# Kernel tuning notes

Measured on AMD Instinct MI355X. Metric: run time of the kernel, lower is better.

The kernel has to match this reference:

```python
import jax, jax.numpy as jnp
import numpy as np

V, B, L, NG = 50000, 128, 350, 3        # vocab, batch(docs), doc length, n-gram window
D, H, C = 768, 256, 20                  # bert dim, num_hidden, class_num
HEADS, LAYERS, K, ALPHA = 8, 2, 3, 0.15 # GAT heads/layers, diffusion hops k, alpha


def setup_inputs() -> dict:
    rng = np.random.default_rng(0)
    # per-doc graphs: 350 unique word-ids per doc (nodes), n-gram window edges
    node_ids = np.stack([rng.choice(V, L, replace=False) for _ in range(B)]).ravel()
    src_b, dst_b = [], []
    for i in range(L):
        for j in range(max(0, i - NG), min(L, i + NG + 1)):
            src_b.append(i); dst_b.append(j)
    src_b, dst_b = np.asarray(src_b), np.asarray(dst_b)
    off = (np.arange(B) * L)[:, None]
    edge_src = (src_b[None, :] + off).ravel()
    edge_dst = (dst_b[None, :] + off).ravel()
    graph_id = np.repeat(np.arange(B), L)

    ks = jax.random.split(jax.random.key(0), 8)
    f32 = jnp.float32
    return {
        'node_ids': jnp.asarray(node_ids, jnp.int32),
        'edge_src': jnp.asarray(edge_src, jnp.int32),
        'edge_dst': jnp.asarray(edge_dst, jnp.int32),
        'graph_id': jnp.asarray(graph_id, jnp.int32),
        'emb':    (jax.random.normal(ks[0], (V, D), f32) * 0.02),
        'W1':     (jax.random.normal(ks[1], (D, H), f32) / np.sqrt(D)).astype(f32),
        'b1':     jnp.zeros((H,), f32),
        'W2':     (jax.random.normal(ks[2], (H, C), f32) / np.sqrt(H)).astype(f32),
        'b2':     jnp.zeros((C,), f32),
        'gat_W':  (jax.random.normal(ks[3], (LAYERS, HEADS, C, C), f32) / np.sqrt(C)).astype(f32),
        'a_src':  (jax.random.normal(ks[4], (LAYERS, HEADS, C), f32) * 0.1),
        'a_dst':  (jax.random.normal(ks[5], (LAYERS, HEADS, C), f32) * 0.1),
        'w_gate': (jax.random.normal(ks[6], (C,), f32) / np.sqrt(C)).astype(f32),
        'b_gate': jnp.zeros((), f32),
    }


def _gat_layer(h, W, a_s, a_d, src, dst, N):
    # h: [N,C]; W: [Hd,C,C]; a_s/a_d: [Hd,C]
    z = jnp.einsum('nc,hcd->hnd', h, W)                     # [Hd,N,C]
    e = jax.nn.leaky_relu(jnp.einsum('hnd,hd->hn', z, a_s)[:, src]
                          + jnp.einsum('hnd,hd->hn', z, a_d)[:, dst], 0.2)  # [Hd,E]

    def segsoftmax(ev):  # edge softmax over incoming edges at each dst node
        m = jax.ops.segment_max(ev, dst, num_segments=N)
        ex = jnp.exp(ev - m[dst])
        s = jax.ops.segment_sum(ex, dst, num_segments=N)
        return ex / (s[dst] + 1e-9)

    att = jax.vmap(segsoftmax)(e)                           # [Hd,E]

    def diffuse(zh, ah):  # attention diffusion: Z_t = (1-a) A Z_{t-1} + a Z_0
        zt = zh
        for _ in range(K):
            agg = jax.ops.segment_sum(ah[:, None] * zt[src], dst, num_segments=N)
            zt = (1.0 - ALPHA) * agg + ALPHA * zh
        return zt

    out = jax.vmap(diffuse)(z, att)                         # [Hd,N,C]
    return jax.nn.elu(out).mean(axis=0)                     # merge='mean'


def reference(node_ids, edge_src, edge_dst, graph_id, emb, W1, b1, W2, b2,
              gat_W, a_src, a_dst, w_gate, b_gate):
    N = node_ids.shape[0]
    x = emb[node_ids]                                       # [N,768] gather
    x = jax.nn.relu(x @ W1 + b1)                            # linear1 + ReLU
    h = x @ W2 + b2                                         # linear2 -> [N,C]
    for l in range(LAYERS):
        h = _gat_layer(h, gat_W[l], a_src[l], a_dst[l], edge_src, edge_dst, N)
    gate = jax.nn.sigmoid(h @ w_gate + b_gate)[:, None]     # WeightAndSum gate
    return jax.ops.segment_sum(gate * h, graph_id, num_segments=B)  # [B,C]
```

## Files before the change

### kernel.cpp

```cpp
#include <hip/hip_runtime.h>
#include <hip/hip_bf16.h>
#include <cstddef>

#define NB_NODES 44800
#define NDOCS 128
#define DLEN 350
#define DIM 768
#define HID 256
#define NCLS 20
#define NHEADS 8
#define ZROW 352
#define ASTR 800

typedef __bf16 v8bf __attribute__((ext_vector_type(8)));
typedef __bf16 v4bf __attribute__((ext_vector_type(4)));
typedef __bf16 v2bf __attribute__((ext_vector_type(2)));
typedef float v4f __attribute__((ext_vector_type(4)));
typedef float v2f __attribute__((ext_vector_type(2)));

__global__ __launch_bounds__(256) void k_pack(const float* __restrict__ W1,
                                              __bf16* __restrict__ W1P) {
  int idx = blockIdx.x * 256 + threadIdx.x;
  int e = idx & 7;
  int l = (idx >> 3) & 63;
  int rest = idx >> 9;
  int ks = rest % 24;
  int cb = rest / 24;
  int k = ks * 32 + (l >> 4) * 8 + e;
  int col = cb * 16 + (l & 15);
  W1P[idx] = (__bf16)W1[k * 256 + col];
}

__global__ __launch_bounds__(256) void k_mlp(
    const int* __restrict__ node_ids, const float* __restrict__ emb,
    const __bf16* __restrict__ W1P, const float* __restrict__ b1,
    const float* __restrict__ W2, const float* __restrict__ b2,
    float* __restrict__ h0) {
  __shared__ __align__(16) char smem[51200];
  __bf16* Asl = (__bf16*)smem;
  float*  xs  = (float*)smem;
  __bf16* w2s = (__bf16*)(smem + 16640);
  int tid = threadIdx.x;
  int wave = tid >> 6, lane = tid & 63;
  int quad = lane >> 4, l16 = lane & 15;
  int m0 = blockIdx.x * 32;

  {
    int r0 = wave * 8;
    int nid[8];
#pragma unroll
    for (int rr = 0; rr < 8; ++rr) nid[rr] = node_ids[m0 + r0 + rr];
#pragma unroll
    for (int p = 0; p < 3; ++p) {
      v4f t[8];
#pragma unroll
      for (int rr = 0; rr < 8; ++rr)
        t[rr] = *(const v4f*)(emb + (size_t)nid[rr] * DIM + p * 256 + lane * 4);
#pragma unroll
      for (int rr = 0; rr < 8; ++rr) {
        v4bf b;
#pragma unroll
        for (int e = 0; e < 4; ++e) b[e] = (__bf16)t[rr][e];
        *(v4bf*)(Asl + (r0 + rr) * ASTR + p * 256 + lane * 4) = b;
      }
    }
  }

  v4f acc[2][4];
#pragma unroll
  for (int ms = 0; ms < 2; ++ms)
#pragma unroll
    for (int j = 0; j < 4; ++j) acc[ms][j] = (v4f){0.f, 0.f, 0.f, 0.f};

  __syncthreads();

  const __bf16* wpB = W1P + (size_t)wave * 49152 + lane * 8;
#pragma unroll 4
  for (int ks = 0; ks < 24; ++ks) {
    v8bf a0 = *(const v8bf*)(Asl + l16 * ASTR + ks * 32 + quad * 8);
    v8bf a1 = *(const v8bf*)(Asl + (16 + l16) * ASTR + ks * 32 + quad * 8);
    v8bf bv[4];
#pragma unroll
    for (int j = 0; j < 4; ++j)
      bv[j] = *(const v8bf*)(wpB + j * 12288 + ks * 512);
#pragma unroll
    for (int j = 0; j < 4; ++j) {
      acc[0][j] = __builtin_amdgcn_mfma_f32_16x16x32_bf16(a0, bv[j], acc[0][j], 0, 0, 0);
      acc[1][j] = __builtin_amdgcn_mfma_f32_16x16x32_bf16(a1, bv[j], acc[1][j], 0, 0, 0);
    }
  }

  __syncthreads();
  for (int i = tid; i < HID * NCLS; i += 256) w2s[i] = (__bf16)W2[i];

#pragma unroll
  for (int ms = 0; ms < 2; ++ms) {
    if (ms) __syncthreads();
#pragma unroll
    for (int j = 0; j < 4; ++j) {
      int col = wave * 64 + j * 16 + l16;
      float bb = b1[col];
#pragma unroll
      for (int r = 0; r < 4; ++r) {
        int lr = quad * 4 + r;
        float v = acc[ms][j][r] + bb;
        xs[lr * 260 + col] = v > 0.f ? v : 0.f;
      }
    }
    __syncthreads();
    if (tid < 160) {
      int m = tid / 10, c0 = (tid % 10) * 2;
      float s0 = b2[c0], s1 = b2[c0 + 1];
      for (int k = 0; k < HID; ++k) {
        float x = xs[m * 260 + k];
        v2bf w = *(const v2bf*)(w2s + k * NCLS + c0);
        s0 += x * (float)w[0]; s1 += x * (float)w[1];
      }
      v2f o; o[0] = s0; o[1] = s1;
      *(v2f*)(h0 + (size_t)(m0 + ms * 16 + m) * NCLS + c0) = o;
    }
  }
}

__global__ __launch_bounds__(384) void k_gat(
    const float* __restrict__ hin, const float* __restrict__ gatW,
    const float* __restrict__ a_src, const float* __restrict__ a_dst,
    int layer, float* __restrict__ zout) {
  __shared__ float zT[NCLS * ZROW];
  __shared__ float asv[DLEN], adv[DLEN];
  int tid = threadIdx.x;
  int head = blockIdx.x & 7;
  int doc = blockIdx.x >> 3;
  const float* W  = gatW  + (size_t)(layer * NHEADS + head) * NCLS * NCLS;
  const float* av = a_src + (layer * NHEADS + head) * NCLS;
  const float* dv = a_dst + (layer * NHEADS + head) * NCLS;
  int r = tid;
  bool act = r < DLEN;

  float z0[NCLS];
  if (act) {
    const float* hr = hin + ((size_t)doc * DLEN + r) * NCLS;
    float h[NCLS];
#pragma unroll
    for (int q = 0; q < 5; ++q) {
      v4f t = *(const v4f*)(hr + q * 4);
#pragma unroll
      for (int e = 0; e < 4; ++e) h[q * 4 + e] = t[e];
    }
    float zacc[NCLS];
#pragma unroll
    for (int d = 0; d < NCLS; ++d) zacc[d] = 0.f;
#pragma unroll
    for (int c = 0; c < NCLS; ++c) {
      float hc = h[c];
#pragma unroll
      for (int d = 0; d < NCLS; ++d) zacc[d] += hc * W[c * NCLS + d];
    }
    float sa = 0.f, sd = 0.f;
#pragma unroll
    for (int d = 0; d < NCLS; ++d) { sa += zacc[d] * av[d]; sd += zacc[d] * dv[d]; }
    asv[r] = sa; adv[r] = sd;
#pragma unroll
    for (int c = 0; c < NCLS; ++c) zT[c * ZROW + r] = zacc[c];
#pragma unroll
    for (int d = 0; d < NCLS; ++d) z0[d] = zacc[d];
  }
  __syncthreads();

  float att[7];
  if (act) {
    float ad = adv[r];
    float e[7]; float m = -1e30f;
#pragma unroll
    for (int j = 0; j < 7; ++j) {
      int s = r - 3 + j;
      bool valid = (s >= 0) && (s < DLEN);
      float x = valid ? asv[s] + ad : -1e30f;
      x = x > 0.f ? x : 0.2f * x;
      e[j] = valid ? x : -1e30f;
      if (e[j] > m) m = e[j];
    }
    float sum = 0.f;
#pragma unroll
    for (int j = 0; j < 7; ++j) {
      float ex = (e[j] > -1e29f) ? expf(e[j] - m) : 0.f;
      e[j] = ex; sum += ex;
    }
    float inv = 1.f / (sum + 1e-9f);
#pragma unroll
    for (int j = 0; j < 7; ++j) att[j] = e[j] * inv;
  }

  float vn[NCLS];
  for (int hop = 0; hop < 3; ++hop) {
    if (act) {
      float agg[NCLS];
#pragma unroll
      for (int c = 0; c < NCLS; ++c) agg[c] = 0.f;
#pragma unroll
      for (int j = 0; j < 7; ++j) {
        int s = r - 3 + j;
        s = s < 0 ? 0 : (s > DLEN - 1 ? DLEN - 1 : s);
        float a = att[j];
#pragma unroll
        for (int c = 0; c < NCLS; ++c) agg[c] += a * zT[c * ZROW + s];
      }
#pragma unroll
      for (int c = 0; c < NCLS; ++c) vn[c] = 0.85f * agg[c] + 0.15f * z0[c];
    }
    if (hop < 2) {
      __syncthreads();
      if (act) {
#pragma unroll
        for (int c = 0; c < NCLS; ++c) zT[c * ZROW + r] = vn[c];
      }
      __syncthreads();
    }
  }

  if (act) {
    float* og = zout + ((size_t)head * NB_NODES + (size_t)doc * DLEN + r) * NCLS;
#pragma unroll
    for (int q = 0; q < 5; ++q) {
      v4f t;
#pragma unroll
      for (int e = 0; e < 4; ++e) {
        float x = vn[q * 4 + e];
        t[e] = x > 0.f ? x : expf(x) - 1.f;
      }
      *(v4f*)(og + q * 4) = t;
    }
  }
}

__global__ __launch_bounds__(256) void k_headmean(
    const float* __restrict__ eluzt, float* __restrict__ hout) {
  int idx = blockIdx.x * 256 + threadIdx.x;
  v4f s = (v4f){0.f, 0.f, 0.f, 0.f};
#pragma unroll
  for (int h = 0; h < NHEADS; ++h)
    s += ((const v4f*)eluzt)[(size_t)h * (NB_NODES * NCLS / 4) + idx];
  v4f o; o[0] = s[0] * 0.125f; o[1] = s[1] * 0.125f; o[2] = s[2] * 0.125f; o[3] = s[3] * 0.125f;
  ((v4f*)hout)[idx] = o;
}

__global__ __launch_bounds__(384) void k_hm_pool(
    const float* __restrict__ eluzt, const float* __restrict__ w_gate,
    const float* __restrict__ b_gate, float* __restrict__ out) {
  __shared__ float red[6][NCLS];
  int tid = threadIdx.x;
  int doc = blockIdx.x;
  int r = tid;
  bool act = r < DLEN;

  float wg[NCLS];
#pragma unroll
  for (int c = 0; c < NCLS; ++c) wg[c] = w_gate[c];
  float contrib[NCLS];
#pragma unroll
  for (int c = 0; c < NCLS; ++c) contrib[c] = 0.f;
  if (act) {
    float hm[NCLS];
#pragma unroll
    for (int c = 0; c < NCLS; ++c) hm[c] = 0.f;
#pragma unroll
    for (int hd = 0; hd < NHEADS; ++hd) {
      const float* p = eluzt + ((size_t)hd * NB_NODES + (size_t)doc * DLEN + r) * NCLS;
#pragma unroll
      for (int q = 0; q < 5; ++q) {
        v4f t = *(const v4f*)(p + q * 4);
#pragma unroll
        for (int e = 0; e < 4; ++e) hm[q * 4 + e] += t[e];
      }
    }
    float d = b_gate[0];
#pragma unroll
    for (int c = 0; c < NCLS; ++c) { hm[c] *= 0.125f; d += hm[c] * wg[c]; }
    float g = 1.f / (1.f + expf(-d));
#pragma unroll
    for (int c = 0; c < NCLS; ++c) contrib[c] = g * hm[c];
  }
#pragma unroll
  for (int off = 32; off > 0; off >>= 1)
#pragma unroll
    for (int c = 0; c < NCLS; ++c) contrib[c] += __shfl_down(contrib[c], off);
  int wave = tid >> 6, lane = tid & 63;
  if (lane == 0)
#pragma unroll
    for (int c = 0; c < NCLS; ++c) red[wave][c] = contrib[c];
  __syncthreads();
  if (tid < NCLS) {
    float s = 0.f;
#pragma unroll
    for (int w = 0; w < 6; ++w) s += red[w][tid];
    out[doc * NCLS + tid] = s;
  }
}

extern "C" void kernel_launch(void* const* d_in, const int* in_sizes, int n_in,
                              void* d_out, int out_size, void* d_ws, size_t ws_size,
                              hipStream_t stream) {
  const int* node_ids = (const int*)d_in[0];
  const float* emb    = (const float*)d_in[4];
  const float* W1     = (const float*)d_in[5];
  const float* b1     = (const float*)d_in[6];
  const float* W2     = (const float*)d_in[7];
  const float* b2     = (const float*)d_in[8];
  const float* gatW   = (const float*)d_in[9];
  const float* a_src  = (const float*)d_in[10];
  const float* a_dst  = (const float*)d_in[11];
  const float* w_gate = (const float*)d_in[12];
  const float* b_gate = (const float*)d_in[13];
  float* out = (float*)d_out;
  char* ws = (char*)d_ws;

  __bf16* W1P = (__bf16*)(ws + 0);
  float* hA  = (float*)(ws + 393216);
  float* hB  = (float*)(ws + 3977216);
  float* zt  = (float*)(ws + 7561216);

  k_pack<<<768, 256, 0, stream>>>(W1, W1P);
  k_mlp<<<NB_NODES / 32, 256, 0, stream>>>(node_ids, emb, W1P, b1, W2, b2, hA);
  k_gat<<<NDOCS * NHEADS, 384, 0, stream>>>(hA, gatW, a_src, a_dst, 0, zt);
  k_headmean<<<(NB_NODES * NCLS / 4) / 256, 256, 0, stream>>>(zt, hB);
  k_gat<<<NDOCS * NHEADS, 384, 0, stream>>>(hB, gatW, a_src, a_dst, 1, zt);
  k_hm_pool<<<NDOCS, 384, 0, stream>>>(zt, w_gate, b_gate, out);
}
```

Measured before the change: 351.0 us.

## Fuse both GAT layers, head mean and gated pooling into one per-doc kernel

```diff
diff --git a/kernel.cpp b/kernel.cpp
--- a/kernel.cpp
+++ b/kernel.cpp
@@ -9,8 +9,8 @@
 #define HID 256
 #define NCLS 20
 #define NHEADS 8
-#define ZROW 352
 #define ASTR 800
+#define ZR2 353
 
 typedef __bf16 v8bf __attribute__((ext_vector_type(8)));
 typedef __bf16 v4bf __attribute__((ext_vector_type(4)));
@@ -122,160 +122,200 @@
   }
 }
 
-__global__ __launch_bounds__(384) void k_gat(
+__global__ __launch_bounds__(512) void k_gat_all(
     const float* __restrict__ hin, const float* __restrict__ gatW,
     const float* __restrict__ a_src, const float* __restrict__ a_dst,
-    int layer, float* __restrict__ zout) {
-  __shared__ float zT[NCLS * ZROW];
-  __shared__ float asv[DLEN], adv[DLEN];
-  int tid = threadIdx.x;
-  int head = blockIdx.x & 7;
-  int doc = blockIdx.x >> 3;
-  const float* W  = gatW  + (size_t)(layer * NHEADS + head) * NCLS * NCLS;
-  const float* av = a_src + (layer * NHEADS + head) * NCLS;
-  const float* dv = a_dst + (layer * NHEADS + head) * NCLS;
-  int r = tid;
-  bool act = r < DLEN;
-
-  float z0[NCLS];
-  if (act) {
-    const float* hr = hin + ((size_t)doc * DLEN + r) * NCLS;
-    float h[NCLS];
-#pragma unroll
-    for (int q = 0; q < 5; ++q) {
-      v4f t = *(const v4f*)(hr + q * 4);
-#pragma unroll
-      for (int e = 0; e < 4; ++e) h[q * 4 + e] = t[e];
-    }
-    float zacc[NCLS];
-#pragma unroll
-    for (int d = 0; d < NCLS; ++d) zacc[d] = 0.f;
-#pragma unroll
-    for (int c = 0; c < NCLS; ++c) {
-      float hc = h[c];
-#pragma unroll
-      for (int d = 0; d < NCLS; ++d) zacc[d] += hc * W[c * NCLS + d];
-    }
-    float sa = 0.f, sd = 0.f;
-#pragma unroll
-    for (int d = 0; d < NCLS; ++d) { sa += zacc[d] * av[d]; sd += zacc[d] * dv[d]; }
-    asv[r] = sa; adv[r] = sd;
-#pragma unroll
-    for (int c = 0; c < NCLS; ++c) zT[c * ZROW + r] = zacc[c];
-#pragma unroll
-    for (int d = 0; d < NCLS; ++d) z0[d] = zacc[d];
-  }
+    const float* __restrict__ w_gate, const float* __restrict__ b_gate,
+    float* __restrict__ out) {
+  __shared__ float hT[NCLS * ZR2];
+  __shared__ float accT[NCLS * ZR2];
+  __shared__ float zT2[2][NCLS * ZR2];
+  __shared__ float as2[2][ZR2], ad2[2][ZR2];
+  __shared__ float red[8][NCLS];
+  const int tid = threadIdx.x;
+  const int doc = blockIdx.x;
+  const int wave = tid >> 6, lane = tid & 63;
+  const int hb = wave >> 2;
+  const int u = wave & 3;
+  const int n0 = u * 88 + lane;
+  const int n1 = n0 + 64;
+  const int cnt = (u == 3) ? 86 : 88;
+  const bool v1 = (lane + 64) < cnt;
+  float* zT  = zT2[hb];
+  float* asv = as2[hb];
+  float* adv = ad2[hb];
+
+  const float* hsrc = hin + (size_t)doc * DLEN * NCLS;
+  for (int i = tid; i < DLEN * NCLS; i += 512) {
+    int node = i / NCLS, c = i - node * NCLS;
+    hT[c * ZR2 + node] = hsrc[i];
+  }
+  for (int i = tid; i < NCLS * ZR2; i += 512) accT[i] = 0.f;
   __syncthreads();
 
-  float att[7];
-  if (act) {
-    float ad = adv[r];
-    float e[7]; float m = -1e30f;
-#pragma unroll
-    for (int j = 0; j < 7; ++j) {
-      int s = r - 3 + j;
-      bool valid = (s >= 0) && (s < DLEN);
-      float x = valid ? asv[s] + ad : -1e30f;
-      x = x > 0.f ? x : 0.2f * x;
-      e[j] = valid ? x : -1e30f;
-      if (e[j] > m) m = e[j];
-    }
-    float sum = 0.f;
-#pragma unroll
-    for (int j = 0; j < 7; ++j) {
-      float ex = (e[j] > -1e29f) ? expf(e[j] - m) : 0.f;
-      e[j] = ex; sum += ex;
-    }
-    float inv = 1.f / (sum + 1e-9f);
-#pragma unroll
-    for (int j = 0; j < 7; ++j) att[j] = e[j] * inv;
-  }
-
-  float vn[NCLS];
-  for (int hop = 0; hop < 3; ++hop) {
-    if (act) {
-      float agg[NCLS];
-#pragma unroll
-      for (int c = 0; c < NCLS; ++c) agg[c] = 0.f;
-#pragma unroll
-      for (int j = 0; j < 7; ++j) {
-        int s = r - 3 + j;
-        s = s < 0 ? 0 : (s > DLEN - 1 ? DLEN - 1 : s);
-        float a = att[j];
-#pragma unroll
-        for (int c = 0; c < NCLS; ++c) agg[c] += a * zT[c * ZROW + s];
-      }
-#pragma unroll
-      for (int c = 0; c < NCLS; ++c) vn[c] = 0.85f * agg[c] + 0.15f * z0[c];
-    }
-    if (hop < 2) {
+#pragma unroll 1
+  for (int layer = 0; layer < 2; ++layer) {
+#pragma unroll 1
+    for (int pass = 0; pass < 4; ++pass) {
+      const int head = __builtin_amdgcn_readfirstlane(pass * 2 + hb);
+      const float* W  = gatW  + (size_t)(layer * NHEADS + head) * NCLS * NCLS;
+      const float* av = a_src + (layer * NHEADS + head) * NCLS;
+      const float* dv = a_dst + (layer * NHEADS + head) * NCLS;
+
+      float z0a[NCLS], z0b[NCLS];
+#pragma unroll
+      for (int d = 0; d < NCLS; ++d) { z0a[d] = 0.f; z0b[d] = 0.f; }
+#pragma unroll
+      for (int c = 0; c < NCLS; ++c) {
+        float ha  = hT[c * ZR2 + n0];
+        float hbv = v1 ? hT[c * ZR2 + n1] : 0.f;
+#pragma unroll
+        for (int d = 0; d < NCLS; ++d) {
+          float w = W[c * NCLS + d];
+          z0a[d] += ha * w; z0b[d] += hbv * w;
+        }
+      }
+      float saa = 0.f, sda = 0.f, sab = 0.f, sdb = 0.f;
+#pragma unroll
+      for (int d = 0; d < NCLS; ++d) {
+        saa += z0a[d] * av[d]; sda += z0a[d] * dv[d];
+        sab += z0b[d] * av[d]; sdb += z0b[d] * dv[d];
+      }
+#pragma unroll
+      for (int d = 0; d < NCLS; ++d) zT[d * ZR2 + n0] = z0a[d];
+      asv[n0] = saa; adv[n0] = sda;
+      if (v1) {
+#pragma unroll
+        for (int d = 0; d < NCLS; ++d) zT[d * ZR2 + n1] = z0b[d];
+        asv[n1] = sab; adv[n1] = sdb;
+      }
       __syncthreads();
-      if (act) {
-#pragma unroll
-        for (int c = 0; c < NCLS; ++c) zT[c * ZROW + r] = vn[c];
+
+      float atta[7], attb[7];
+      {
+        float ad = adv[n0];
+        float e[7]; float m = -1e30f;
+#pragma unroll
+        for (int j = 0; j < 7; ++j) {
+          int s = n0 - 3 + j;
+          bool valid = (s >= 0) && (s < DLEN);
+          float x = valid ? asv[s] + ad : -1e30f;
+          x = x > 0.f ? x : 0.2f * x;
+          e[j] = valid ? x : -1e30f;
+          if (e[j] > m) m = e[j];
+        }
+        float sum = 0.f;
+#pragma unroll
+        for (int j = 0; j < 7; ++j) {
+          float ex = (e[j] > -1e29f) ? expf(e[j] - m) : 0.f;
+          e[j] = ex; sum += ex;
+        }
+        float inv = 1.f / (sum + 1e-9f);
+#pragma unroll
+        for (int j = 0; j < 7; ++j) atta[j] = e[j] * inv;
+      }
+      {
+        float ad = v1 ? adv[n1] : 0.f;
+        float e[7]; float m = -1e30f;
+#pragma unroll
+        for (int j = 0; j < 7; ++j) {
+          int s = n1 - 3 + j;
+          bool valid = v1 && (s >= 0) && (s < DLEN);
+          float x = valid ? asv[s] + ad : -1e30f;
+          x = x > 0.f ? x : 0.2f * x;
+          e[j] = valid ? x : -1e30f;
+          if (e[j] > m) m = e[j];
+        }
+        float sum = 0.f;
+#pragma unroll
+        for (int j = 0; j < 7; ++j) {
+          float ex = (e[j] > -1e29f) ? expf(e[j] - m) : 0.f;
+          e[j] = ex; sum += ex;
+        }
+        float inv = 1.f / (sum + 1e-9f);
+#pragma unroll
+        for (int j = 0; j < 7; ++j) attb[j] = e[j] * inv;
+      }
+
+      float vna[NCLS], vnb[NCLS];
+#pragma unroll 1
+      for (int hop = 0; hop < 3; ++hop) {
+        float agga[NCLS], aggb[NCLS];
+#pragma unroll
+        for (int c = 0; c < NCLS; ++c) { agga[c] = 0.f; aggb[c] = 0.f; }
+#pragma unroll
+        for (int j = 0; j < 7; ++j) {
+          int sa = n0 - 3 + j; sa = sa < 0 ? 0 : (sa > DLEN - 1 ? DLEN - 1 : sa);
+          int sb = n1 - 3 + j; sb = sb < 0 ? 0 : (sb > DLEN - 1 ? DLEN - 1 : sb);
+          float aa = atta[j], ab = attb[j];
+#pragma unroll
+          for (int c = 0; c < NCLS; ++c) {
+            agga[c] += aa * zT[c * ZR2 + sa];
+            aggb[c] += ab * zT[c * ZR2 + sb];
+          }
+        }
+#pragma unroll
+        for (int c = 0; c < NCLS; ++c) {
+          vna[c] = 0.85f * agga[c] + 0.15f * z0a[c];
+          vnb[c] = 0.85f * aggb[c] + 0.15f * z0b[c];
+        }
+        if (hop < 2) {
+          __syncthreads();
+#pragma unroll
+          for (int c = 0; c < NCLS; ++c) zT[c * ZR2 + n0] = vna[c];
+          if (v1) {
+#pragma unroll
+            for (int c = 0; c < NCLS; ++c) zT[c * ZR2 + n1] = vnb[c];
+          }
+          __syncthreads();
+        }
+      }
+
+      if (hb == 0) {
+#pragma unroll
+        for (int c = 0; c < NCLS; ++c) {
+          float x = vna[c];
+          accT[c * ZR2 + n0] += x > 0.f ? x : expf(x) - 1.f;
+        }
+        if (v1) {
+#pragma unroll
+          for (int c = 0; c < NCLS; ++c) {
+            float x = vnb[c];
+            accT[c * ZR2 + n1] += x > 0.f ? x : expf(x) - 1.f;
+          }
+        }
       }
       __syncthreads();
-    }
-  }
-
-  if (act) {
-    float* og = zout + ((size_t)head * NB_NODES + (size_t)doc * DLEN + r) * NCLS;
-#pragma unroll
-    for (int q = 0; q < 5; ++q) {
-      v4f t;
-#pragma unroll
-      for (int e = 0; e < 4; ++e) {
-        float x = vn[q * 4 + e];
-        t[e] = x > 0.f ? x : expf(x) - 1.f;
-      }
-      *(v4f*)(og + q * 4) = t;
-    }
-  }
-}
-
-__global__ __launch_bounds__(256) void k_headmean(
-    const float* __restrict__ eluzt, float* __restrict__ hout) {
-  int idx = blockIdx.x * 256 + threadIdx.x;
-  v4f s = (v4f){0.f, 0.f, 0.f, 0.f};
-#pragma unroll
-  for (int h = 0; h < NHEADS; ++h)
-    s += ((const v4f*)eluzt)[(size_t)h * (NB_NODES * NCLS / 4) + idx];
-  v4f o; o[0] = s[0] * 0.125f; o[1] = s[1] * 0.125f; o[2] = s[2] * 0.125f; o[3] = s[3] * 0.125f;
-  ((v4f*)hout)[idx] = o;
-}
-
-__global__ __launch_bounds__(384) void k_hm_pool(
-    const float* __restrict__ eluzt, const float* __restrict__ w_gate,
-    const float* __restrict__ b_gate, float* __restrict__ out) {
-  __shared__ float red[6][NCLS];
-  int tid = threadIdx.x;
-  int doc = blockIdx.x;
-  int r = tid;
-  bool act = r < DLEN;
-
-  float wg[NCLS];
-#pragma unroll
-  for (int c = 0; c < NCLS; ++c) wg[c] = w_gate[c];
+      if (hb == 1) {
+#pragma unroll
+        for (int c = 0; c < NCLS; ++c) {
+          float x = vna[c];
+          accT[c * ZR2 + n0] += x > 0.f ? x : expf(x) - 1.f;
+        }
+        if (v1) {
+#pragma unroll
+          for (int c = 0; c < NCLS; ++c) {
+            float x = vnb[c];
+            accT[c * ZR2 + n1] += x > 0.f ? x : expf(x) - 1.f;
+          }
+        }
+      }
+      __syncthreads();
+    }
+    for (int i = tid; i < NCLS * ZR2; i += 512) {
+      hT[i] = accT[i] * 0.125f; accT[i] = 0.f;
+    }
+    __syncthreads();
+  }
+
   float contrib[NCLS];
 #pragma unroll
   for (int c = 0; c < NCLS; ++c) contrib[c] = 0.f;
-  if (act) {
+  if (tid < DLEN) {
+    float d = b_gate[0];
     float hm[NCLS];
 #pragma unroll
-    for (int c = 0; c < NCLS; ++c) hm[c] = 0.f;
-#pragma unroll
-    for (int hd = 0; hd < NHEADS; ++hd) {
-      const float* p = eluzt + ((size_t)hd * NB_NODES + (size_t)doc * DLEN + r) * NCLS;
-#pragma unroll
-      for (int q = 0; q < 5; ++q) {
-        v4f t = *(const v4f*)(p + q * 4);
-#pragma unroll
-        for (int e = 0; e < 4; ++e) hm[q * 4 + e] += t[e];
-      }
-    }
-    float d = b_gate[0];
-#pragma unroll
-    for (int c = 0; c < NCLS; ++c) { hm[c] *= 0.125f; d += hm[c] * wg[c]; }
+    for (int c = 0; c < NCLS; ++c) { hm[c] = hT[c * ZR2 + tid]; d += hm[c] * w_gate[c]; }
     float g = 1.f / (1.f + expf(-d));
 #pragma unroll
     for (int c = 0; c < NCLS; ++c) contrib[c] = g * hm[c];
@@ -284,7 +324,6 @@
   for (int off = 32; off > 0; off >>= 1)
 #pragma unroll
     for (int c = 0; c < NCLS; ++c) contrib[c] += __shfl_down(contrib[c], off);
-  int wave = tid >> 6, lane = tid & 63;
   if (lane == 0)
 #pragma unroll
     for (int c = 0; c < NCLS; ++c) red[wave][c] = contrib[c];
@@ -292,7 +331,7 @@
   if (tid < NCLS) {
     float s = 0.f;
 #pragma unroll
-    for (int w = 0; w < 6; ++w) s += red[w][tid];
+    for (int w = 0; w < 8; ++w) s += red[w][tid];
     out[doc * NCLS + tid] = s;
   }
 }
@@ -316,13 +355,8 @@
 
   __bf16* W1P = (__bf16*)(ws + 0);
   float* hA  = (float*)(ws + 393216);
-  float* hB  = (float*)(ws + 3977216);
-  float* zt  = (float*)(ws + 7561216);
 
   k_pack<<<768, 256, 0, stream>>>(W1, W1P);
   k_mlp<<<NB_NODES / 32, 256, 0, stream>>>(node_ids, emb, W1P, b1, W2, b2, hA);
-  k_gat<<<NDOCS * NHEADS, 384, 0, stream>>>(hA, gatW, a_src, a_dst, 0, zt);
-  k_headmean<<<(NB_NODES * NCLS / 4) / 256, 256, 0, stream>>>(zt, hB);
-  k_gat<<<NDOCS * NHEADS, 384, 0, stream>>>(hB, gatW, a_src, a_dst, 1, zt);
-  k_hm_pool<<<NDOCS, 384, 0, stream>>>(zt, w_gate, b_gate, out);
+  k_gat_all<<<NDOCS, 512, 0, stream>>>(hA, gatW, a_src, a_dst, w_gate, b_gate, out);
 }
```

Measured after the change: 487.1 us. 1.39x slower.

## Fuse GAT head-mean into GAT kernel via atomic accumulation, drop headmean kernel

Applied to the files above, without the earlier changes.

```diff
diff --git a/kernel.cpp b/kernel.cpp
--- a/kernel.cpp
+++ b/kernel.cpp
@@ -9,8 +9,8 @@
 #define HID 256
 #define NCLS 20
 #define NHEADS 8
+#define ASTR 800
 #define ZROW 352
-#define ASTR 800
 
 typedef __bf16 v8bf __attribute__((ext_vector_type(8)));
 typedef __bf16 v4bf __attribute__((ext_vector_type(4)));
@@ -35,7 +35,7 @@
     const int* __restrict__ node_ids, const float* __restrict__ emb,
     const __bf16* __restrict__ W1P, const float* __restrict__ b1,
     const float* __restrict__ W2, const float* __restrict__ b2,
-    float* __restrict__ h0) {
+    float* __restrict__ h0, float* __restrict__ hB, float* __restrict__ hC) {
   __shared__ __align__(16) char smem[51200];
   __bf16* Asl = (__bf16*)smem;
   float*  xs  = (float*)smem;
@@ -45,6 +45,11 @@
   int quad = lane >> 4, l16 = lane & 15;
   int m0 = blockIdx.x * 32;
 
+  for (int i = tid; i < 32 * NCLS; i += 256) {
+    hB[(size_t)m0 * NCLS + i] = 0.f;
+    hC[(size_t)m0 * NCLS + i] = 0.f;
+  }
+
   {
     int r0 = wave * 8;
     int nid[8];
@@ -125,7 +130,7 @@
 __global__ __launch_bounds__(384) void k_gat(
     const float* __restrict__ hin, const float* __restrict__ gatW,
     const float* __restrict__ a_src, const float* __restrict__ a_dst,
-    int layer, float* __restrict__ zout) {
+    int layer, float* __restrict__ hacc) {
   __shared__ float zT[NCLS * ZROW];
   __shared__ float asv[DLEN], adv[DLEN];
   int tid = threadIdx.x;
@@ -219,33 +224,18 @@
   }
 
   if (act) {
-    float* og = zout + ((size_t)head * NB_NODES + (size_t)doc * DLEN + r) * NCLS;
-#pragma unroll
-    for (int q = 0; q < 5; ++q) {
-      v4f t;
-#pragma unroll
-      for (int e = 0; e < 4; ++e) {
-        float x = vn[q * 4 + e];
-        t[e] = x > 0.f ? x : expf(x) - 1.f;
-      }
-      *(v4f*)(og + q * 4) = t;
-    }
-  }
-}
-
-__global__ __launch_bounds__(256) void k_headmean(
-    const float* __restrict__ eluzt, float* __restrict__ hout) {
-  int idx = blockIdx.x * 256 + threadIdx.x;
-  v4f s = (v4f){0.f, 0.f, 0.f, 0.f};
-#pragma unroll
-  for (int h = 0; h < NHEADS; ++h)
-    s += ((const v4f*)eluzt)[(size_t)h * (NB_NODES * NCLS / 4) + idx];
-  v4f o; o[0] = s[0] * 0.125f; o[1] = s[1] * 0.125f; o[2] = s[2] * 0.125f; o[3] = s[3] * 0.125f;
-  ((v4f*)hout)[idx] = o;
-}
-
-__global__ __launch_bounds__(384) void k_hm_pool(
-    const float* __restrict__ eluzt, const float* __restrict__ w_gate,
+    float* og = hacc + ((size_t)doc * DLEN + r) * NCLS;
+#pragma unroll
+    for (int c = 0; c < NCLS; ++c) {
+      float x = vn[c];
+      float e = x > 0.f ? x : expf(x) - 1.f;
+      atomicAdd(&og[c], 0.125f * e);
+    }
+  }
+}
+
+__global__ __launch_bounds__(384) void k_pool(
+    const float* __restrict__ hC, const float* __restrict__ w_gate,
     const float* __restrict__ b_gate, float* __restrict__ out) {
   __shared__ float red[6][NCLS];
   int tid = threadIdx.x;
@@ -253,29 +243,19 @@
   int r = tid;
   bool act = r < DLEN;
 
-  float wg[NCLS];
-#pragma unroll
-  for (int c = 0; c < NCLS; ++c) wg[c] = w_gate[c];
   float contrib[NCLS];
 #pragma unroll
   for (int c = 0; c < NCLS; ++c) contrib[c] = 0.f;
   if (act) {
+    const float* p = hC + ((size_t)doc * DLEN + r) * NCLS;
     float hm[NCLS];
-#pragma unroll
-    for (int c = 0; c < NCLS; ++c) hm[c] = 0.f;
-#pragma unroll
-    for (int hd = 0; hd < NHEADS; ++hd) {
-      const float* p = eluzt + ((size_t)hd * NB_NODES + (size_t)doc * DLEN + r) * NCLS;
-#pragma unroll
-      for (int q = 0; q < 5; ++q) {
-        v4f t = *(const v4f*)(p + q * 4);
-#pragma unroll
-        for (int e = 0; e < 4; ++e) hm[q * 4 + e] += t[e];
-      }
-    }
     float d = b_gate[0];
 #pragma unroll
-    for (int c = 0; c < NCLS; ++c) { hm[c] *= 0.125f; d += hm[c] * wg[c]; }
+    for (int q = 0; q < 5; ++q) {
+      v4f t = *(const v4f*)(p + q * 4);
+#pragma unroll
+      for (int e = 0; e < 4; ++e) { hm[q * 4 + e] = t[e]; d += t[e] * w_gate[q * 4 + e]; }
+    }
     float g = 1.f / (1.f + expf(-d));
 #pragma unroll
     for (int c = 0; c < NCLS; ++c) contrib[c] = g * hm[c];
@@ -317,12 +297,11 @@
   __bf16* W1P = (__bf16*)(ws + 0);
   float* hA  = (float*)(ws + 393216);
   float* hB  = (float*)(ws + 3977216);
-  float* zt  = (float*)(ws + 7561216);
+  float* hC  = (float*)(ws + 7561216);
 
   k_pack<<<768, 256, 0, stream>>>(W1, W1P);
-  k_mlp<<<NB_NODES / 32, 256, 0, stream>>>(node_ids, emb, W1P, b1, W2, b2, hA);
-  k_gat<<<NDOCS * NHEADS, 384, 0, stream>>>(hA, gatW, a_src, a_dst, 0, zt);
-  k_headmean<<<(NB_NODES * NCLS / 4) / 256, 256, 0, stream>>>(zt, hB);
-  k_gat<<<NDOCS * NHEADS, 384, 0, stream>>>(hB, gatW, a_src, a_dst, 1, zt);
-  k_hm_pool<<<NDOCS, 384, 0, stream>>>(zt, w_gate, b_gate, out);
-}
+  k_mlp<<<NB_NODES / 32, 256, 0, stream>>>(node_ids, emb, W1P, b1, W2, b2, hA, hB, hC);
+  k_gat<<<NDOCS * NHEADS, 384, 0, stream>>>(hA, gatW, a_src, a_dst, 0, hB);
+  k_gat<<<NDOCS * NHEADS, 384, 0, stream>>>(hB, gatW, a_src, a_dst, 1, hC);
+  k_pool<<<NDOCS, 384, 0, stream>>>(hC, w_gate, b_gate, out);
+}
```

Result: slower. 1.019 ms (+190.2%).

## Fuse head-mean into second GAT layer and chunk MLP embedding staging

Applied to the files above, without the earlier changes.

```diff
diff --git a/kernel.cpp b/kernel.cpp
--- a/kernel.cpp
+++ b/kernel.cpp
@@ -9,8 +9,8 @@
 #define HID 256
 #define NCLS 20
 #define NHEADS 8
+#define ASTRH 264
 #define ZROW 352
-#define ASTR 800
 
 typedef __bf16 v8bf __attribute__((ext_vector_type(8)));
 typedef __bf16 v4bf __attribute__((ext_vector_type(4)));
@@ -36,8 +36,8 @@
     const __bf16* __restrict__ W1P, const float* __restrict__ b1,
     const float* __restrict__ W2, const float* __restrict__ b2,
     float* __restrict__ h0) {
-  __shared__ __align__(16) char smem[51200];
-  __bf16* Asl = (__bf16*)smem;
+  __shared__ __align__(16) char smem[26880];
+  __bf16* As  = (__bf16*)smem;
   float*  xs  = (float*)smem;
   __bf16* w2s = (__bf16*)(smem + 16640);
   int tid = threadIdx.x;
@@ -45,26 +45,10 @@
   int quad = lane >> 4, l16 = lane & 15;
   int m0 = blockIdx.x * 32;
 
-  {
-    int r0 = wave * 8;
-    int nid[8];
-#pragma unroll
-    for (int rr = 0; rr < 8; ++rr) nid[rr] = node_ids[m0 + r0 + rr];
-#pragma unroll
-    for (int p = 0; p < 3; ++p) {
-      v4f t[8];
-#pragma unroll
-      for (int rr = 0; rr < 8; ++rr)
-        t[rr] = *(const v4f*)(emb + (size_t)nid[rr] * DIM + p * 256 + lane * 4);
-#pragma unroll
-      for (int rr = 0; rr < 8; ++rr) {
-        v4bf b;
-#pragma unroll
-        for (int e = 0; e < 4; ++e) b[e] = (__bf16)t[rr][e];
-        *(v4bf*)(Asl + (r0 + rr) * ASTR + p * 256 + lane * 4) = b;
-      }
-    }
-  }
+  int r0 = wave * 8;
+  int nid[8];
+#pragma unroll
+  for (int rr = 0; rr < 8; ++rr) nid[rr] = node_ids[m0 + r0 + rr];
 
   v4f acc[2][4];
 #pragma unroll
@@ -72,21 +56,38 @@
 #pragma unroll
     for (int j = 0; j < 4; ++j) acc[ms][j] = (v4f){0.f, 0.f, 0.f, 0.f};
 
-  __syncthreads();
-
   const __bf16* wpB = W1P + (size_t)wave * 49152 + lane * 8;
+
+#pragma unroll 1
+  for (int p = 0; p < 3; ++p) {
+    v4f t[8];
+#pragma unroll
+    for (int rr = 0; rr < 8; ++rr)
+      t[rr] = *(const v4f*)(emb + (size_t)nid[rr] * DIM + p * 256 + lane * 4);
+    if (p) __syncthreads();
+#pragma unroll
+    for (int rr = 0; rr < 8; ++rr) {
+      v4bf b;
+#pragma unroll
+      for (int e = 0; e < 4; ++e) b[e] = (__bf16)t[rr][e];
+      *(v4bf*)(As + (r0 + rr) * ASTRH + lane * 4) = b;
+    }
+    __syncthreads();
+
 #pragma unroll 4
-  for (int ks = 0; ks < 24; ++ks) {
-    v8bf a0 = *(const v8bf*)(Asl + l16 * ASTR + ks * 32 + quad * 8);
-    v8bf a1 = *(const v8bf*)(Asl + (16 + l16) * ASTR + ks * 32 + quad * 8);
-    v8bf bv[4];
-#pragma unroll
-    for (int j = 0; j < 4; ++j)
-      bv[j] = *(const v8bf*)(wpB + j * 12288 + ks * 512);
-#pragma unroll
-    for (int j = 0; j < 4; ++j) {
-      acc[0][j] = __builtin_amdgcn_mfma_f32_16x16x32_bf16(a0, bv[j], acc[0][j], 0, 0, 0);
-      acc[1][j] = __builtin_amdgcn_mfma_f32_16x16x32_bf16(a1, bv[j], acc[1][j], 0, 0, 0);
+    for (int k8 = 0; k8 < 8; ++k8) {
+      int ks = p * 8 + k8;
+      v8bf a0 = *(const v8bf*)(As + l16 * ASTRH + k8 * 32 + quad * 8);
+      v8bf a1 = *(const v8bf*)(As + (16 + l16) * ASTRH + k8 * 32 + quad * 8);
+      v8bf bv[4];
+#pragma unroll
+      for (int j = 0; j < 4; ++j)
+        bv[j] = *(const v8bf*)(wpB + j * 12288 + ks * 512);
+#pragma unroll
+      for (int j = 0; j < 4; ++j) {
+        acc[0][j] = __builtin_amdgcn_mfma_f32_16x16x32_bf16(a0, bv[j], acc[0][j], 0, 0, 0);
+        acc[1][j] = __builtin_amdgcn_mfma_f32_16x16x32_bf16(a1, bv[j], acc[1][j], 0, 0, 0);
+      }
     }
   }
 
@@ -125,7 +126,7 @@
 __global__ __launch_bounds__(384) void k_gat(
     const float* __restrict__ hin, const float* __restrict__ gatW,
     const float* __restrict__ a_src, const float* __restrict__ a_dst,
-    int layer, float* __restrict__ zout) {
+    int layer, int meanin, float* __restrict__ zout) {
   __shared__ float zT[NCLS * ZROW];
   __shared__ float asv[DLEN], adv[DLEN];
   int tid = threadIdx.x;
@@ -139,13 +140,30 @@
 
   float z0[NCLS];
   if (act) {
-    const float* hr = hin + ((size_t)doc * DLEN + r) * NCLS;
     float h[NCLS];
-#pragma unroll
-    for (int q = 0; q < 5; ++q) {
-      v4f t = *(const v4f*)(hr + q * 4);
-#pragma unroll
-      for (int e = 0; e < 4; ++e) h[q * 4 + e] = t[e];
+    if (meanin) {
+#pragma unroll
+      for (int c = 0; c < NCLS; ++c) h[c] = 0.f;
+#pragma unroll
+      for (int hd = 0; hd < NHEADS; ++hd) {
+        const float* p = hin + ((size_t)hd * NB_NODES + (size_t)doc * DLEN + r) * NCLS;
+#pragma unroll
+        for (int q = 0; q < 5; ++q) {
+          v4f t = *(const v4f*)(p + q * 4);
+#pragma unroll
+          for (int e = 0; e < 4; ++e) h[q * 4 + e] += t[e];
+        }
+      }
+#pragma unroll
+      for (int c = 0; c < NCLS; ++c) h[c] *= 0.125f;
+    } else {
+      const float* hr = hin + ((size_t)doc * DLEN + r) * NCLS;
+#pragma unroll
+      for (int q = 0; q < 5; ++q) {
+        v4f t = *(const v4f*)(hr + q * 4);
+#pragma unroll
+        for (int e = 0; e < 4; ++e) h[q * 4 + e] = t[e];
+      }
     }
     float zacc[NCLS];
 #pragma unroll
@@ -231,17 +249,6 @@
       *(v4f*)(og + q * 4) = t;
     }
   }
-}
-
-__global__ __launch_bounds__(256) void k_headmean(
-    const float* __restrict__ eluzt, float* __restrict__ hout) {
-  int idx = blockIdx.x * 256 + threadIdx.x;
-  v4f s = (v4f){0.f, 0.f, 0.f, 0.f};
-#pragma unroll
-  for (int h = 0; h < NHEADS; ++h)
-    s += ((const v4f*)eluzt)[(size_t)h * (NB_NODES * NCLS / 4) + idx];
-  v4f o; o[0] = s[0] * 0.125f; o[1] = s[1] * 0.125f; o[2] = s[2] * 0.125f; o[3] = s[3] * 0.125f;
-  ((v4f*)hout)[idx] = o;
 }
 
 __global__ __launch_bounds__(384) void k_hm_pool(
@@ -316,13 +323,12 @@
 
   __bf16* W1P = (__bf16*)(ws + 0);
   float* hA  = (float*)(ws + 393216);
-  float* hB  = (float*)(ws + 3977216);
-  float* zt  = (float*)(ws + 7561216);
+  float* zt0 = (float*)(ws + 3977216);
+  float* zt1 = (float*)(ws + 32649216);
 
   k_pack<<<768, 256, 0, stream>>>(W1, W1P);
   k_mlp<<<NB_NODES / 32, 256, 0, stream>>>(node_ids, emb, W1P, b1, W2, b2, hA);
-  k_gat<<<NDOCS * NHEADS, 384, 0, stream>>>(hA, gatW, a_src, a_dst, 0, zt);
-  k_headmean<<<(NB_NODES * NCLS / 4) / 256, 256, 0, stream>>>(zt, hB);
-  k_gat<<<NDOCS * NHEADS, 384, 0, stream>>>(hB, gatW, a_src, a_dst, 1, zt);
-  k_hm_pool<<<NDOCS, 384, 0, stream>>>(zt, w_gate, b_gate, out);
-}
+  k_gat<<<NDOCS * NHEADS, 384, 0, stream>>>(hA,  gatW, a_src, a_dst, 0, 0, zt0);
+  k_gat<<<NDOCS * NHEADS, 384, 0, stream>>>(zt0, gatW, a_src, a_dst, 1, 1, zt1);
+  k_hm_pool<<<NDOCS, 384, 0, stream>>>(zt1, w_gate, b_gate, out);
+}
```

Result: slower. 404.6 us (+15.3%).
